# Performance work log

Hardware: AMD Instinct MI355X
Metric: run time of the kernel (lower is better)

Reference implementation:

```python
import jax, jax.numpy as jnp
import numpy as np

T = 1_000_000          # number of t_eval points (~1 year at 30 s)
N_ROOMS = 10
N = 12                 # 2 latent wall nodes + n_rooms
DT = 30.0              # seconds between t_eval points
LOAD_SCALE = 50.0      # physical_cooling_scaling: W/m^2 scale for sigmoid(loads)


def setup_inputs() -> dict:
    key = jax.random.key(0)
    k1, k2, k3, k4, k5 = jax.random.split(key, 5)
    t_eval = jnp.arange(T, dtype=jnp.float32) * DT
    x0 = 26.0 * jnp.ones((N,), jnp.float32)  # reset_iv: 26 C at every node
    # Stable slow RC dynamics: negative-definite-ish A with small coupling
    A = (-1e-5 * jnp.eye(N, dtype=jnp.float32)
         + 1e-6 * jax.random.normal(k1, (N, N), jnp.float32))
    B = 1e-6 * jax.random.normal(k2, (N, 1 + N_ROOMS), jnp.float32)
    Tout_data = 10.0 + 20.0 * jax.random.uniform(k3, (T,), jnp.float32)  # outdoor temp samples on t_eval grid
    loads_raw = jax.random.normal(k4, (2, N_ROOMS), jnp.float32)         # pre-sigmoid [cool; gain] loads
    room_areas = 10.0 + 40.0 * jax.random.uniform(k5, (N_ROOMS,), jnp.float32)
    return {"t_eval": t_eval, "x0": x0, "A": A, "B": B,
            "Tout_data": Tout_data, "loads_raw": loads_raw, "room_areas": room_areas}


def reference(t_eval, x0, A, B, Tout_data, loads_raw, room_areas):
    # transform + physical scaling of loads (self.transform = sigmoid)
    loads = jax.nn.sigmoid(loads_raw) * LOAD_SCALE
    cool_load, gain_load = loads[0], loads[1]
    action = 0.0  # no cooling policy -> self.action stays 0
    Q_area = -cool_load * action + gain_load            # [n_rooms]
    Q_watts = Q_area * room_areas                        # proportional_heating
    # u = [Tout; Q_watts] so B@u = B[:,0]*Tout + B[:,1:]@Q_watts (Q constant over t)
    b0 = B[:, 0]                                         # [N]
    Bq = B[:, 1:] @ Q_watts                              # [N], constant forcing
    h = t_eval[1] - t_eval[0]                            # uniform step
    # Linear interp of Tout: value at t_i, midpoint t_i+h/2, and t_{i+1}
    To_t = Tout_data[:-1]
    To_n = Tout_data[1:]
    To_m = 0.5 * (To_t + To_n)

    def f(x, To):  # dy/dt = A x + B u
        return A @ x + b0 * To + Bq

    def step(x, tou):
        to_t, to_m, to_n = tou
        k1 = f(x, to_t)
        k2 = f(x + 0.5 * h * k1, to_m)
        k3 = f(x + 0.5 * h * k2, to_m)
        k4 = f(x + h * k3, to_n)
        xn = x + (h / 6.0) * (k1 + 2.0 * k2 + 2.0 * k3 + k4)
        return xn, xn

    _, xs = jax.lax.scan(step, x0, (To_t, To_m, To_n))
    return jnp.concatenate([x0[None, :], xs], axis=0)  # [T, N]
```

## Files before the change

### kernel.cpp

```cpp
#include <hip/hip_runtime.h>
#include <math.h>


#define S_STEPS 999999
#define CH      8
#define BLK     512
#define NB      256
#define NLOOK   16
#define NCHUNK  125000
#define LASTFULL 124998

#define OFF_M   0
#define OFF_C   144
#define OFF_AL  156
#define OFF_BE  168
#define OFF_K   192
#define OFF_P2  312
#define OFF_PQ  1608
#define OFF_PW  2040
#define OFF_PD  3048
#define OFF_AGG 5352

#define FMA4(Q,a,b,c,d,acc) fmaf((Q).w,(d),fmaf((Q).z,(c),fmaf((Q).y,(b),fmaf((Q).x,(a),(acc)))))

__device__ __forceinline__ void mv_acc(const float* Pf, const float* x, float* y) {
  const float4* P = reinterpret_cast<const float4*>(Pf);
#pragma unroll
  for (int i = 0; i < 12; ++i) {
    float4 a = P[3*i], b = P[3*i+1], c = P[3*i+2];
    y[i] = FMA4(c, x[8],x[9],x[10],x[11],
            FMA4(b, x[4],x[5],x[6],x[7],
             FMA4(a, x[0],x[1],x[2],x[3], y[i])));
  }
}

__device__ __forceinline__ void fold_chunk(const float* cons, const float* tos, float* v) {
  const float4* Kq = reinterpret_cast<const float4*>(cons + OFF_K);
  float4 c0=Kq[0], c1=Kq[1], c2=Kq[2];
  v[0]=c0.x; v[1]=c0.y; v[2]=c0.z; v[3]=c0.w;
  v[4]=c1.x; v[5]=c1.y; v[6]=c1.z; v[7]=c1.w;
  v[8]=c2.x; v[9]=c2.y; v[10]=c2.z; v[11]=c2.w;
#pragma unroll
  for (int s = 0; s < 9; ++s) {
    float ts = tos[s];
    float4 ka=Kq[3*(s+1)], kb=Kq[3*(s+1)+1], kc=Kq[3*(s+1)+2];
    v[0]=fmaf(ka.x,ts,v[0]); v[1]=fmaf(ka.y,ts,v[1]); v[2]=fmaf(ka.z,ts,v[2]); v[3]=fmaf(ka.w,ts,v[3]);
    v[4]=fmaf(kb.x,ts,v[4]); v[5]=fmaf(kb.y,ts,v[5]); v[6]=fmaf(kb.z,ts,v[6]); v[7]=fmaf(kb.w,ts,v[7]);
    v[8]=fmaf(kc.x,ts,v[8]); v[9]=fmaf(kc.y,ts,v[9]); v[10]=fmaf(kc.z,ts,v[10]); v[11]=fmaf(kc.w,ts,v[11]);
  }
}

__global__ void __launch_bounds__(512) setup_kernel(
    const float* __restrict__ t_eval, const float* __restrict__ A,
    const float* __restrict__ Bm, const float* __restrict__ loads_raw,
    const float* __restrict__ areas, float* ws) {
  __shared__ double H1[144], H2[144], H3[144], H4[144], Md[144];
  __shared__ double Qa[144], Qb[144], D1536[144];
  __shared__ double C128[144], C256[144], C512[144], C1024[144], C2048[144], C4096[144];
  __shared__ double cd[12], ald[12], bed[12], b0d[12], bqd[12];
  __shared__ double Vv[3][12], Kd[120];
  int t = threadIdx.x;
  double h = (double)t_eval[1] - (double)t_eval[0];
  if (t < 144) H1[t] = h * (double)A[t];
  if (t < 12) {
    b0d[t] = (double)Bm[t*11];
    double s = 0.0;
    for (int r = 0; r < 10; ++r) {
      double gq = 50.0 / (1.0 + exp(-(double)loads_raw[10 + r]));
      s += (double)Bm[t*11 + 1 + r] * (gq * (double)areas[r]);
    }
    bqd[t] = s;
  }
  if (t < 120) Kd[t] = 0.0;
  __syncthreads();
  if (t < 144) {
    int i=t/12, j=t%12; double s=0.0;
#pragma unroll
    for (int m = 0; m < 12; ++m) s += H1[i*12+m]*H1[m*12+j];
    H2[t]=s;
  }
  __syncthreads();
  if (t < 288) {
    int w=t/144, e=t%144, i=e/12, j=e%12;
    const double* Bp = w ? H2 : H1;
    double s = 0.0;
#pragma unroll
    for (int m = 0; m < 12; ++m) s += H2[i*12+m]*Bp[m*12+j];
    (w ? H4 : H3)[e] = s;
  }
  __syncthreads();
  if (t < 12) {
    double hb=0,h2b=0,h3b=0,hb0=0,h2b0=0,h3b0=0;
#pragma unroll
    for (int m = 0; m < 12; ++m) {
      hb  += H1[t*12+m]*bqd[m]; h2b  += H2[t*12+m]*bqd[m]; h3b  += H3[t*12+m]*bqd[m];
      hb0 += H1[t*12+m]*b0d[m]; h2b0 += H2[t*12+m]*b0d[m]; h3b0 += H3[t*12+m]*b0d[m];
    }
    double h6 = h / 6.0;
    cd[t]  = h6*(6.0*bqd[t] + 3.0*hb + h2b + 0.25*h3b);
    ald[t] = h6*(3.0*b0d[t] + 2.0*hb0 + 0.75*h2b0 + 0.25*h3b0);
    bed[t] = h6*(3.0*b0d[t] + hb0 + 0.25*h2b0);
    Vv[0][t]=ald[t]; Vv[1][t]=bed[t]; Vv[2][t]=cd[t];
    Kd[96+t] += ald[t]; Kd[108+t] += bed[t]; Kd[t] += cd[t];
  }
  if (t >= 144 && t < 288) {
    int e=t-144, i=e/12, j=e%12;
    Md[e] = (i==j ? 1.0 : 0.0) + H1[e] + 0.5*H2[e] + H3[e]/6.0 + H4[e]/24.0;
  }
  __syncthreads();
  if (t < 144) { ws[OFF_M+t] = (float)Md[t]; Qa[t] = Md[t]; }
  if (t < 12) {
    ws[OFF_C+t]=(float)cd[t]; ws[OFF_AL+t]=(float)ald[t]; ws[OFF_BE+t]=(float)bed[t];
  }
  __syncthreads();
  double* src = Qa; double* dst = Qb;
  for (int r = 1; r <= 12; ++r) {
    double acc = 0.0, ks = 0.0;
    if (t < 144) {
      int i=t/12, j=t%12;
#pragma unroll
      for (int m = 0; m < 12; ++m) acc += src[i*12+m]*src[m*12+j];
    }
    int w=0, i2=0;
    if (r <= 7 && t >= 256 && t < 292) {
      w=(t-256)/12; i2=(t-256)%12;
#pragma unroll
      for (int m = 0; m < 12; ++m) ks += Md[i2*12+m]*Vv[w][m];
    }
    __syncthreads();
    if (t < 144) {
      dst[t] = acc;
      if (r >= 3 && r <= 11) ws[OFF_P2+(r-3)*144+t] = (float)acc;
      if (r == 7)  C128[t]=acc;
      if (r == 8)  C256[t]=acc;
      if (r == 9)  C512[t]=acc;
      if (r == 10) C1024[t]=acc;
      if (r == 11) C2048[t]=acc;
      if (r == 12) C4096[t]=acc;
    }
    if (r <= 7 && t >= 256 && t < 292) {
      Vv[w][i2] = ks;
      if (w == 0) Kd[(8-r)*12+i2] += ks;
      else if (w == 1) Kd[(9-r)*12+i2] += ks;
      else Kd[i2] += ks;
    }
    __syncthreads();
    double* tmp = src; src = dst; dst = tmp;
  }
  if (t < 120) ws[OFF_K+t] = (float)Kd[t];
  if (t < 144) {
    ws[OFF_PQ+t]       = (float)C128[t];
    ws[OFF_PQ+144+t]   = (float)C256[t];
    ws[OFF_PW+t]       = (float)C512[t];
    ws[OFF_PW+144+t]   = (float)C1024[t];
    ws[OFF_PW+3*144+t] = (float)C2048[t];
    ws[OFF_PD+t]       = (t % 13 == 0) ? 1.f : 0.f;
    ws[OFF_PD+144+t]   = (float)C4096[t];
  }
  if (t < 432) {
    int w=t/144, e=t%144, i=e/12, j=e%12;
    const double* Ap = (w==0) ? C128 : C512;
    const double* Bp = (w==0) ? C256 : ((w==1) ? C1024 : C2048);
    double s = 0.0;
#pragma unroll
    for (int m = 0; m < 12; ++m) s += Ap[i*12+m]*Bp[m*12+j];
    if (w==0) ws[OFF_PQ+2*144+e] = (float)s;
    else if (w==1) { D1536[e]=s; ws[OFF_PW+2*144+e] = (float)s; }
    else ws[OFF_PW+4*144+e] = (float)s;
  }
  __syncthreads();
  if (t < 288) {
    int w=t/144, e=t%144, i=e/12, j=e%12;
    const double* Ap = (w==0) ? C1024 : D1536;
    double s = 0.0;
#pragma unroll
    for (int m = 0; m < 12; ++m) s += Ap[i*12+m]*C2048[m*12+j];
    ws[OFF_PW+((w==0)?5:6)*144+e] = (float)s;
  }
  for (int j = 2; j < NLOOK; ++j) {
    double acc = 0.0;
    if (t < 144) {
      int i=t/12, jj=t%12;
#pragma unroll
      for (int m = 0; m < 12; ++m) acc += src[i*12+m]*C4096[m*12+jj];
    }
    __syncthreads();
    if (t < 144) { dst[t] = acc; ws[OFF_PD+j*144+t] = (float)acc; }
    __syncthreads();
    double* tmp = src; src = dst; dst = tmp;
  }
}

__global__ void __launch_bounds__(BLK) block_agg(
    const float* cons, const float* __restrict__ To,
    const float* __restrict__ x0, float* agg) {
  __shared__ float Tw[96], Ta[48], Tb[24];
  int k = threadIdx.x, b = blockIdx.x;
  int g = b*BLK + k, base = g*CH;
  float v[12];
  if (g <= LASTFULL) {
    const float4* tp = reinterpret_cast<const float4*>(To + base);
    float4 ta = tp[0], tb = tp[1];
    float tos[9] = {ta.x,ta.y,ta.z,ta.w, tb.x,tb.y,tb.z,tb.w, To[base+8]};
    fold_chunk(cons, tos, v);
  } else {
#pragma unroll
    for (int i = 0; i < 12; ++i) v[i] = 0.f;
  }
  if (g == 0) {
    float xi[12];
#pragma unroll
    for (int i = 0; i < 12; ++i) xi[i] = x0[i];
    mv_acc(cons + OFF_P2, xi, v);
  }
#pragma unroll
  for (int l = 0; l < 6; ++l) {
    int off = 1 << l;
    float nb[12];
#pragma unroll
    for (int i = 0; i < 12; ++i) nb[i] = __shfl_up(v[i], (unsigned)off, 64);
    if ((k & 63) >= off) mv_acc(cons + OFF_P2 + l*144, nb, v);
  }
  if ((k & 63) == 63) {
#pragma unroll
    for (int i = 0; i < 12; ++i) Tw[(k>>6)*12 + i] = v[i];
  }
  __syncthreads();
  if (k < 48) {
    int p = k/12, i = k%12;
    const float* L = Tw + 2*p*12;
    float acc = Tw[(2*p+1)*12 + i];
    const float4* Pr = reinterpret_cast<const float4*>(cons + OFF_P2 + 6*144 + i*12);
    float4 p0=Pr[0], p1=Pr[1], p2=Pr[2];
    acc = FMA4(p0, L[0],L[1],L[2],L[3], acc);
    acc = FMA4(p1, L[4],L[5],L[6],L[7], acc);
    acc = FMA4(p2, L[8],L[9],L[10],L[11], acc);
    Ta[p*12+i] = acc;
  }
  __syncthreads();
  if (k < 24) {
    int q = k/12, i = k%12;
    const float* L = Ta + 2*q*12;
    float acc = Ta[(2*q+1)*12 + i];
    const float4* Pr = reinterpret_cast<const float4*>(cons + OFF_P2 + 7*144 + i*12);
    float4 p0=Pr[0], p1=Pr[1], p2=Pr[2];
    acc = FMA4(p0, L[0],L[1],L[2],L[3], acc);
    acc = FMA4(p1, L[4],L[5],L[6],L[7], acc);
    acc = FMA4(p2, L[8],L[9],L[10],L[11], acc);
    Tb[q*12+i] = acc;
  }
  __syncthreads();
  if (k < 12) {
    float acc = Tb[12 + k];
    const float4* Pr = reinterpret_cast<const float4*>(cons + OFF_P2 + 8*144 + k*12);
    float4 p0=Pr[0], p1=Pr[1], p2=Pr[2];
    acc = FMA4(p0, Tb[0],Tb[1],Tb[2],Tb[3], acc);
    acc = FMA4(p1, Tb[4],Tb[5],Tb[6],Tb[7], acc);
    acc = FMA4(p2, Tb[8],Tb[9],Tb[10],Tb[11], acc);
    agg[b*12 + k] = acc;
  }
}

#define ROWX(i, MA,MB,MC) xn[i] = FMA4(MC, x[8],x[9],x[10],x[11], \
    FMA4(MB, x[4],x[5],x[6],x[7], FMA4(MA, x[0],x[1],x[2],x[3], \
    fmaf(bv[i],ton,fmaf(av[i],tot,cv[i])))));

__global__ void __launch_bounds__(BLK, 2) scan_expand(
    const float* cons, const float* __restrict__ To,
    const float* __restrict__ x0, float* __restrict__ out) {
  __shared__ float lw[BLK*13];
  __shared__ float partl[NLOOK*12];
  __shared__ float Xs[12];
  __shared__ float Xw[96];
  __shared__ float Xq[384];
  int k = threadIdx.x, b = blockIdx.x;
  int g = b*BLK + k, base = g*CH;
  bool active = (g < NCHUNK), fullc = (g <= LASTFULL);
  float to[9];
  if (active) {
    const float4* tp = reinterpret_cast<const float4*>(To + base);
    float4 ta = tp[0], tb = tp[1];
    to[0]=ta.x; to[1]=ta.y; to[2]=ta.z; to[3]=ta.w;
    to[4]=tb.x; to[5]=tb.y; to[6]=tb.z; to[7]=tb.w;
    to[8] = fullc ? To[base+8] : 0.f;
  }
  float v[12];
  if (fullc) fold_chunk(cons, to, v);
  else {
#pragma unroll
    for (int i = 0; i < 12; ++i) v[i] = 0.f;
  }
  if (g == 0) {
    float xi[12];
#pragma unroll
    for (int i = 0; i < 12; ++i) xi[i] = x0[i];
    mv_acc(cons + OFF_P2, xi, v);
  }
#pragma unroll
  for (int i = 0; i < 12; ++i) lw[k*13+i] = v[i];
  if (k < NLOOK*12) {
    int j = k/12, i = k%12, src = b - 1 - j;
    float acc = 0.f;
    if (src >= 0) {
      const float4* Pr = reinterpret_cast<const float4*>(cons + OFF_PD + j*144 + i*12);
      const float4* Ar = reinterpret_cast<const float4*>(cons + OFF_AGG + src*12);
      float4 p0=Pr[0], p1=Pr[1], p2=Pr[2], a0=Ar[0], a1=Ar[1], a2=Ar[2];
      acc = FMA4(p0, a0.x,a0.y,a0.z,a0.w, acc);
      acc = FMA4(p1, a1.x,a1.y,a1.z,a1.w, acc);
      acc = FMA4(p2, a2.x,a2.y,a2.z,a2.w, acc);
    }
    partl[k] = acc;
  }
  __syncthreads();
  if (k < 12) {
    float s = 0.f;
#pragma unroll
    for (int j = 0; j < NLOOK; ++j) s += partl[j*12 + k];
    Xs[k] = s;
  }
#pragma unroll
  for (int l = 0; l < 9; ++l) {
    int off = 1 << l;
    bool act = (k >= off);
    float nb[12];
    if (act) {
#pragma unroll
      for (int i = 0; i < 12; ++i) nb[i] = lw[(k-off)*13 + i];
    }
    __syncthreads();
    if (act) {
      mv_acc(cons + OFF_P2 + l*144, nb, v);
#pragma unroll
      for (int i = 0; i < 12; ++i) lw[k*13+i] = v[i];
    }
    __syncthreads();
  }
  float sp[12];
  if (k > 0) {
#pragma unroll
    for (int i = 0; i < 12; ++i) sp[i] = lw[(k-1)*13 + i];
  } else {
#pragma unroll
    for (int i = 0; i < 12; ++i) sp[i] = 0.f;
  }
  if (k < 96) {
    int w = k/12, i = k%12;
    float acc;
    if (w == 0) acc = Xs[i];
    else {
      const float4* Wr = reinterpret_cast<const float4*>(cons + OFF_PW + (w-1)*144 + i*12);
      float4 p0=Wr[0], p1=Wr[1], p2=Wr[2];
      acc = FMA4(p0, Xs[0],Xs[1],Xs[2],Xs[3], 0.f);
      acc = FMA4(p1, Xs[4],Xs[5],Xs[6],Xs[7], acc);
      acc = FMA4(p2, Xs[8],Xs[9],Xs[10],Xs[11], acc);
    }
    Xw[w*12 + i] = acc;
  }
  __syncthreads();
  if (k < 384) {
    int q = k/12, i = k%12, d = q & 3;
    const float* xw = Xw + (q>>2)*12;
    float acc;
    if (d == 0) acc = xw[i];
    else {
      const float4* Qr = reinterpret_cast<const float4*>(cons + OFF_PQ + (d-1)*144 + i*12);
      float4 p0=Qr[0], p1=Qr[1], p2=Qr[2];
      acc = FMA4(p0, xw[0],xw[1],xw[2],xw[3], 0.f);
      acc = FMA4(p1, xw[4],xw[5],xw[6],xw[7], acc);
      acc = FMA4(p2, xw[8],xw[9],xw[10],xw[11], acc);
    }
    Xq[q*12 + i] = acc;
  }
  __syncthreads();
  float vp[12];
  {
    const float* xq = Xq + (k>>4)*12;
#pragma unroll
    for (int i = 0; i < 12; ++i) vp[i] = xq[i];
  }
#pragma unroll
  for (int l = 0; l < 4; ++l) {
    if ((k >> l) & 1) {
      float vn[12];
#pragma unroll
      for (int i = 0; i < 12; ++i) vn[i] = 0.f;
      mv_acc(cons + OFF_P2 + l*144, vp, vn);
#pragma unroll
      for (int i = 0; i < 12; ++i) vp[i] = vn[i];
    }
  }
  float x[12];
  if (k > 0) {
#pragma unroll
    for (int i = 0; i < 12; ++i) x[i] = vp[i] + sp[i];
  } else {
#pragma unroll
    for (int i = 0; i < 12; ++i) x[i] = vp[i] + (b == 0 ? x0[i] : 0.f);
  }
  if (b == 0 && k == 0) {
#pragma unroll
    for (int i = 0; i < 12; ++i) out[i] = x0[i];
  }
  if (!active) return;
  float cv[12], av[12], bv[12];
  {
    const float4* Cq = reinterpret_cast<const float4*>(cons + OFF_C);
    const float4* Aq = reinterpret_cast<const float4*>(cons + OFF_AL);
    const float4* Bq = reinterpret_cast<const float4*>(cons + OFF_BE);
    float4 q;
    q=Cq[0]; cv[0]=q.x;cv[1]=q.y;cv[2]=q.z;cv[3]=q.w;
    q=Cq[1]; cv[4]=q.x;cv[5]=q.y;cv[6]=q.z;cv[7]=q.w;
    q=Cq[2]; cv[8]=q.x;cv[9]=q.y;cv[10]=q.z;cv[11]=q.w;
    q=Aq[0]; av[0]=q.x;av[1]=q.y;av[2]=q.z;av[3]=q.w;
    q=Aq[1]; av[4]=q.x;av[5]=q.y;av[6]=q.z;av[7]=q.w;
    q=Aq[2]; av[8]=q.x;av[9]=q.y;av[10]=q.z;av[11]=q.w;
    q=Bq[0]; bv[0]=q.x;bv[1]=q.y;bv[2]=q.z;bv[3]=q.w;
    q=Bq[1]; bv[4]=q.x;bv[5]=q.y;bv[6]=q.z;bv[7]=q.w;
    q=Bq[2]; bv[8]=q.x;bv[9]=q.y;bv[10]=q.z;bv[11]=q.w;
  }
  const float4* Mq = reinterpret_cast<const float4*>(cons + OFF_M);
  float4 m00=Mq[0],  m01=Mq[1],  m02=Mq[2],  m03=Mq[3],  m04=Mq[4],  m05=Mq[5];
  float4 m06=Mq[6],  m07=Mq[7],  m08=Mq[8],  m09=Mq[9],  m10=Mq[10], m11=Mq[11];
  float4 m12=Mq[12], m13=Mq[13], m14=Mq[14], m15=Mq[15], m16=Mq[16], m17=Mq[17];
  float4 m18=Mq[18], m19=Mq[19], m20=Mq[20], m21=Mq[21], m22=Mq[22], m23=Mq[23];
  float4 m24=Mq[24], m25=Mq[25], m26=Mq[26], m27=Mq[27], m28=Mq[28], m29=Mq[29];
  float4 m30=Mq[30], m31=Mq[31], m32=Mq[32], m33=Mq[33], m34=Mq[34], m35=Mq[35];
#pragma unroll
  for (int s = 0; s < CH; ++s) {
    int tt = base + s;
    if (tt >= S_STEPS) break;
    float tot = to[s], ton = to[s+1];
    float xn[12];
    ROWX(0,  m00,m01,m02)  ROWX(1,  m03,m04,m05)
    ROWX(2,  m06,m07,m08)  ROWX(3,  m09,m10,m11)
    ROWX(4,  m12,m13,m14)  ROWX(5,  m15,m16,m17)
    ROWX(6,  m18,m19,m20)  ROWX(7,  m21,m22,m23)
    ROWX(8,  m24,m25,m26)  ROWX(9,  m27,m28,m29)
    ROWX(10, m30,m31,m32)  ROWX(11, m33,m34,m35)
    float4* op = reinterpret_cast<float4*>(out + (size_t)(tt+1)*12);
    op[0] = make_float4(xn[0],xn[1],xn[2],xn[3]);
    op[1] = make_float4(xn[4],xn[5],xn[6],xn[7]);
    op[2] = make_float4(xn[8],xn[9],xn[10],xn[11]);
#pragma unroll
    for (int i = 0; i < 12; ++i) x[i] = xn[i];
  }
}

extern "C" void kernel_launch(void* const* d_in, const int* in_sizes, int n_in,
                              void* d_out, int out_size, void* d_ws, size_t ws_size,
                              hipStream_t stream) {
  const float* t_eval    = (const float*)d_in[0];
  const float* x0        = (const float*)d_in[1];
  const float* A         = (const float*)d_in[2];
  const float* B         = (const float*)d_in[3];
  const float* To        = (const float*)d_in[4];
  const float* loads_raw = (const float*)d_in[5];
  const float* areas     = (const float*)d_in[6];
  float* out = (float*)d_out;
  float* ws  = (float*)d_ws;

  setup_kernel<<<1, 512, 0, stream>>>(t_eval, A, B, loads_raw, areas, ws);
  block_agg<<<NB, BLK, 0, stream>>>(ws, To, x0, ws + OFF_AGG);
  scan_expand<<<NB, BLK, 0, stream>>>(ws, To, x0, out);
}
```

Before: 135.6 us.

## Restructure scan into smaller chunks, more blocks, and wave-shuffle scan

```diff
diff --git a/kernel.cpp b/kernel.cpp
--- a/kernel.cpp
+++ b/kernel.cpp
@@ -3,23 +3,22 @@
 
 
 #define S_STEPS 999999
-#define CH      8
-#define BLK     512
-#define NB      256
-#define NLOOK   16
-#define NCHUNK  125000
-#define LASTFULL 124998
+#define CH      4
+#define BLK     256
+#define NB      977
+#define NCHUNK  250000
+#define LASTFULL 249998
 
 #define OFF_M   0
 #define OFF_C   144
 #define OFF_AL  156
 #define OFF_BE  168
 #define OFF_K   192
-#define OFF_P2  312
-#define OFF_PQ  1608
-#define OFF_PW  2040
-#define OFF_PD  3048
-#define OFF_AGG 5352
+#define OFF_P2  264
+#define OFF_PA  1416
+#define OFF_PL  1704
+#define OFF_PD  2136
+#define OFF_AGG 4440
 
 #define FMA4(Q,a,b,c,d,acc) fmaf((Q).w,(d),fmaf((Q).z,(c),fmaf((Q).y,(b),fmaf((Q).x,(a),(acc)))))
 
@@ -34,14 +33,23 @@
   }
 }
 
-__device__ __forceinline__ void fold_chunk(const float* cons, const float* tos, float* v) {
+__device__ __forceinline__ float rowdot(const float* Prow, const float* xv) {
+  const float4* P = reinterpret_cast<const float4*>(Prow);
+  float4 a = P[0], b = P[1], c = P[2];
+  return FMA4(c, xv[8],xv[9],xv[10],xv[11],
+          FMA4(b, xv[4],xv[5],xv[6],xv[7],
+           FMA4(a, xv[0],xv[1],xv[2],xv[3], 0.f)));
+}
+
+__device__ __forceinline__ void fold_chunk(const float* __restrict__ cons,
+                                           const float* tos, float* v) {
   const float4* Kq = reinterpret_cast<const float4*>(cons + OFF_K);
   float4 c0=Kq[0], c1=Kq[1], c2=Kq[2];
   v[0]=c0.x; v[1]=c0.y; v[2]=c0.z; v[3]=c0.w;
   v[4]=c1.x; v[5]=c1.y; v[6]=c1.z; v[7]=c1.w;
   v[8]=c2.x; v[9]=c2.y; v[10]=c2.z; v[11]=c2.w;
 #pragma unroll
-  for (int s = 0; s < 9; ++s) {
+  for (int s = 0; s < 5; ++s) {
     float ts = tos[s];
     float4 ka=Kq[3*(s+1)], kb=Kq[3*(s+1)+1], kc=Kq[3*(s+1)+2];
     v[0]=fmaf(ka.x,ts,v[0]); v[1]=fmaf(ka.y,ts,v[1]); v[2]=fmaf(ka.z,ts,v[2]); v[3]=fmaf(ka.w,ts,v[3]);
@@ -55,10 +63,11 @@
     const float* __restrict__ Bm, const float* __restrict__ loads_raw,
     const float* __restrict__ areas, float* ws) {
   __shared__ double H1[144], H2[144], H3[144], H4[144], Md[144];
-  __shared__ double Qa[144], Qb[144], D1536[144];
-  __shared__ double C128[144], C256[144], C512[144], C1024[144], C2048[144], C4096[144];
+  __shared__ double Qa[144], Qb[144];
+  __shared__ double C64[144], C128[144], C256[144], C512[144];
+  __shared__ double C1024[144], C2048[144], C4096[144];
   __shared__ double cd[12], ald[12], bed[12], b0d[12], bqd[12];
-  __shared__ double Vv[3][12], Kd[120];
+  __shared__ double Vv[3][12], Kd[72];
   int t = threadIdx.x;
   double h = (double)t_eval[1] - (double)t_eval[0];
   if (t < 144) H1[t] = h * (double)A[t];
@@ -71,7 +80,7 @@
     }
     bqd[t] = s;
   }
-  if (t < 120) Kd[t] = 0.0;
+  if (t < 72) Kd[t] = 0.0;
   __syncthreads();
   if (t < 144) {
     int i=t/12, j=t%12; double s=0.0;
@@ -101,7 +110,7 @@
     ald[t] = h6*(3.0*b0d[t] + 2.0*hb0 + 0.75*h2b0 + 0.25*h3b0);
     bed[t] = h6*(3.0*b0d[t] + hb0 + 0.25*h2b0);
     Vv[0][t]=ald[t]; Vv[1][t]=bed[t]; Vv[2][t]=cd[t];
-    Kd[96+t] += ald[t]; Kd[108+t] += bed[t]; Kd[t] += cd[t];
+    Kd[48+t] += ald[t]; Kd[60+t] += bed[t]; Kd[t] += cd[t];
   }
   if (t >= 144 && t < 288) {
     int e=t-144, i=e/12, j=e%12;
@@ -122,7 +131,7 @@
       for (int m = 0; m < 12; ++m) acc += src[i*12+m]*src[m*12+j];
     }
     int w=0, i2=0;
-    if (r <= 7 && t >= 256 && t < 292) {
+    if (r <= 3 && t >= 256 && t < 292) {
       w=(t-256)/12; i2=(t-256)%12;
 #pragma unroll
       for (int m = 0; m < 12; ++m) ks += Md[i2*12+m]*Vv[w][m];
@@ -130,7 +139,8 @@
     __syncthreads();
     if (t < 144) {
       dst[t] = acc;
-      if (r >= 3 && r <= 11) ws[OFF_P2+(r-3)*144+t] = (float)acc;
+      if (r >= 2 && r <= 9) ws[OFF_P2+(r-2)*144+t] = (float)acc;
+      if (r == 6)  C64[t]=acc;
       if (r == 7)  C128[t]=acc;
       if (r == 8)  C256[t]=acc;
       if (r == 9)  C512[t]=acc;
@@ -138,46 +148,34 @@
       if (r == 11) C2048[t]=acc;
       if (r == 12) C4096[t]=acc;
     }
-    if (r <= 7 && t >= 256 && t < 292) {
+    if (r <= 3 && t >= 256 && t < 292) {
       Vv[w][i2] = ks;
-      if (w == 0) Kd[(8-r)*12+i2] += ks;
-      else if (w == 1) Kd[(9-r)*12+i2] += ks;
+      if (w == 0) Kd[(4-r)*12+i2] += ks;
+      else if (w == 1) Kd[(5-r)*12+i2] += ks;
       else Kd[i2] += ks;
     }
     __syncthreads();
     double* tmp = src; src = dst; dst = tmp;
   }
-  if (t < 120) ws[OFF_K+t] = (float)Kd[t];
+  if (t < 72) ws[OFF_K+t] = (float)Kd[t];
   if (t < 144) {
-    ws[OFF_PQ+t]       = (float)C128[t];
-    ws[OFF_PQ+144+t]   = (float)C256[t];
-    ws[OFF_PW+t]       = (float)C512[t];
-    ws[OFF_PW+144+t]   = (float)C1024[t];
-    ws[OFF_PW+3*144+t] = (float)C2048[t];
-    ws[OFF_PD+t]       = (t % 13 == 0) ? 1.f : 0.f;
-    ws[OFF_PD+144+t]   = (float)C4096[t];
+    ws[OFF_PL+t]     = (float)C1024[t];
+    ws[OFF_PL+144+t] = (float)C2048[t];
+    ws[OFF_PD+t]     = (t % 13 == 0) ? 1.f : 0.f;
+    ws[OFF_PD+144+t] = (float)C4096[t];
   }
   if (t < 432) {
     int w=t/144, e=t%144, i=e/12, j=e%12;
-    const double* Ap = (w==0) ? C128 : C512;
-    const double* Bp = (w==0) ? C256 : ((w==1) ? C1024 : C2048);
+    const double* Ap = (w==0) ? C64 : ((w==1) ? C256 : C1024);
+    const double* Bp = (w==0) ? C128 : ((w==1) ? C512 : C2048);
     double s = 0.0;
 #pragma unroll
     for (int m = 0; m < 12; ++m) s += Ap[i*12+m]*Bp[m*12+j];
-    if (w==0) ws[OFF_PQ+2*144+e] = (float)s;
-    else if (w==1) { D1536[e]=s; ws[OFF_PW+2*144+e] = (float)s; }
-    else ws[OFF_PW+4*144+e] = (float)s;
-  }
-  __syncthreads();
-  if (t < 288) {
-    int w=t/144, e=t%144, i=e/12, j=e%12;
-    const double* Ap = (w==0) ? C1024 : D1536;
-    double s = 0.0;
-#pragma unroll
-    for (int m = 0; m < 12; ++m) s += Ap[i*12+m]*C2048[m*12+j];
-    ws[OFF_PW+((w==0)?5:6)*144+e] = (float)s;
-  }
-  for (int j = 2; j < NLOOK; ++j) {
+    if (w==0) ws[OFF_PA+e] = (float)s;
+    else if (w==1) ws[OFF_PA+144+e] = (float)s;
+    else ws[OFF_PL+2*144+e] = (float)s;
+  }
+  for (int j = 2; j < 16; ++j) {
     double acc = 0.0;
     if (t < 144) {
       int i=t/12, jj=t%12;
@@ -191,19 +189,25 @@
   }
 }
 
-__global__ void __launch_bounds__(BLK) block_agg(
-    const float* cons, const float* __restrict__ To,
-    const float* __restrict__ x0, float* agg) {
-  __shared__ float Tw[96], Ta[48], Tb[24];
+__global__ void __launch_bounds__(BLK, 4) block_agg(
+    const float* __restrict__ cons, const float* __restrict__ To,
+    const float* __restrict__ x0, float* __restrict__ agg) {
+  __shared__ __align__(16) float Tw[48], Ta[24];
   int k = threadIdx.x, b = blockIdx.x;
   int g = b*BLK + k, base = g*CH;
+  bool fullc = (g <= LASTFULL);
+  float to_[5];
+#pragma unroll
+  for (int i = 0; i < 5; ++i) to_[i] = 0.f;
+  if (fullc) {
+    const float4* tp = reinterpret_cast<const float4*>(To + base);
+    float4 ta = tp[0];
+    to_[0]=ta.x; to_[1]=ta.y; to_[2]=ta.z; to_[3]=ta.w;
+    to_[4]=To[base+4];
+  }
   float v[12];
-  if (g <= LASTFULL) {
-    const float4* tp = reinterpret_cast<const float4*>(To + base);
-    float4 ta = tp[0], tb = tp[1];
-    float tos[9] = {ta.x,ta.y,ta.z,ta.w, tb.x,tb.y,tb.z,tb.w, To[base+8]};
-    fold_chunk(cons, tos, v);
-  } else {
+  if (fullc) fold_chunk(cons, to_, v);
+  else {
 #pragma unroll
     for (int i = 0; i < 12; ++i) v[i] = 0.f;
   }
@@ -213,79 +217,56 @@
     for (int i = 0; i < 12; ++i) xi[i] = x0[i];
     mv_acc(cons + OFF_P2, xi, v);
   }
+  int j = k & 63;
 #pragma unroll
   for (int l = 0; l < 6; ++l) {
     int off = 1 << l;
     float nb[12];
 #pragma unroll
     for (int i = 0; i < 12; ++i) nb[i] = __shfl_up(v[i], (unsigned)off, 64);
-    if ((k & 63) >= off) mv_acc(cons + OFF_P2 + l*144, nb, v);
-  }
-  if ((k & 63) == 63) {
+    if (j >= off) mv_acc(cons + OFF_P2 + l*144, nb, v);
+  }
+  if (j == 63) {
 #pragma unroll
     for (int i = 0; i < 12; ++i) Tw[(k>>6)*12 + i] = v[i];
   }
   __syncthreads();
-  if (k < 48) {
-    int p = k/12, i = k%12;
-    const float* L = Tw + 2*p*12;
-    float acc = Tw[(2*p+1)*12 + i];
-    const float4* Pr = reinterpret_cast<const float4*>(cons + OFF_P2 + 6*144 + i*12);
-    float4 p0=Pr[0], p1=Pr[1], p2=Pr[2];
-    acc = FMA4(p0, L[0],L[1],L[2],L[3], acc);
-    acc = FMA4(p1, L[4],L[5],L[6],L[7], acc);
-    acc = FMA4(p2, L[8],L[9],L[10],L[11], acc);
-    Ta[p*12+i] = acc;
-  }
-  __syncthreads();
   if (k < 24) {
-    int q = k/12, i = k%12;
-    const float* L = Ta + 2*q*12;
-    float acc = Ta[(2*q+1)*12 + i];
-    const float4* Pr = reinterpret_cast<const float4*>(cons + OFF_P2 + 7*144 + i*12);
-    float4 p0=Pr[0], p1=Pr[1], p2=Pr[2];
-    acc = FMA4(p0, L[0],L[1],L[2],L[3], acc);
-    acc = FMA4(p1, L[4],L[5],L[6],L[7], acc);
-    acc = FMA4(p2, L[8],L[9],L[10],L[11], acc);
-    Tb[q*12+i] = acc;
+    int p = k/12, comp = k - p*12;
+    Ta[k] = rowdot(cons + OFF_P2 + 6*144 + comp*12, Tw + 2*p*12)
+          + Tw[(2*p+1)*12 + comp];
   }
   __syncthreads();
   if (k < 12) {
-    float acc = Tb[12 + k];
-    const float4* Pr = reinterpret_cast<const float4*>(cons + OFF_P2 + 8*144 + k*12);
-    float4 p0=Pr[0], p1=Pr[1], p2=Pr[2];
-    acc = FMA4(p0, Tb[0],Tb[1],Tb[2],Tb[3], acc);
-    acc = FMA4(p1, Tb[4],Tb[5],Tb[6],Tb[7], acc);
-    acc = FMA4(p2, Tb[8],Tb[9],Tb[10],Tb[11], acc);
-    agg[b*12 + k] = acc;
-  }
-}
-
-#define ROWX(i, MA,MB,MC) xn[i] = FMA4(MC, x[8],x[9],x[10],x[11], \
-    FMA4(MB, x[4],x[5],x[6],x[7], FMA4(MA, x[0],x[1],x[2],x[3], \
-    fmaf(bv[i],ton,fmaf(av[i],tot,cv[i])))));
+    agg[b*12 + k] = rowdot(cons + OFF_P2 + 7*144 + k*12, Ta) + Ta[12 + k];
+  }
+}
 
 __global__ void __launch_bounds__(BLK, 2) scan_expand(
-    const float* cons, const float* __restrict__ To,
-    const float* __restrict__ x0, float* __restrict__ out) {
-  __shared__ float lw[BLK*13];
-  __shared__ float partl[NLOOK*12];
-  __shared__ float Xs[12];
-  __shared__ float Xw[96];
-  __shared__ float Xq[384];
+    const float* __restrict__ cons, const float* __restrict__ To,
+    const float* __restrict__ x0, const float* __restrict__ agg,
+    float* __restrict__ out) {
+  __shared__ __align__(16) float Tw[48];
+  __shared__ __align__(16) float Pw[48];
+  __shared__ __align__(16) float lkb[64*12];
+  __shared__ __align__(16) float yv[16*12];
+  __shared__ __align__(16) float zv[16*12];
+  __shared__ __align__(16) float Xs[12];
+  __shared__ __align__(16) float Qw[48];
   int k = threadIdx.x, b = blockIdx.x;
   int g = b*BLK + k, base = g*CH;
   bool active = (g < NCHUNK), fullc = (g <= LASTFULL);
-  float to[9];
+  float to_[5];
+#pragma unroll
+  for (int i = 0; i < 5; ++i) to_[i] = 0.f;
   if (active) {
     const float4* tp = reinterpret_cast<const float4*>(To + base);
-    float4 ta = tp[0], tb = tp[1];
-    to[0]=ta.x; to[1]=ta.y; to[2]=ta.z; to[3]=ta.w;
-    to[4]=tb.x; to[5]=tb.y; to[6]=tb.z; to[7]=tb.w;
-    to[8] = fullc ? To[base+8] : 0.f;
+    float4 ta = tp[0];
+    to_[0]=ta.x; to_[1]=ta.y; to_[2]=ta.z; to_[3]=ta.w;
+    to_[4] = fullc ? To[base+4] : 0.f;
   }
   float v[12];
-  if (fullc) fold_chunk(cons, to, v);
+  if (fullc) fold_chunk(cons, to_, v);
   else {
 #pragma unroll
     for (int i = 0; i < 12; ++i) v[i] = 0.f;
@@ -296,151 +277,127 @@
     for (int i = 0; i < 12; ++i) xi[i] = x0[i];
     mv_acc(cons + OFF_P2, xi, v);
   }
-#pragma unroll
-  for (int i = 0; i < 12; ++i) lw[k*13+i] = v[i];
-  if (k < NLOOK*12) {
-    int j = k/12, i = k%12, src = b - 1 - j;
+  int j = k & 63, w = k >> 6;
+#pragma unroll
+  for (int l = 0; l < 6; ++l) {
+    int off = 1 << l;
+    float nb[12];
+#pragma unroll
+    for (int i = 0; i < 12; ++i) nb[i] = __shfl_up(v[i], (unsigned)off, 64);
+    if (j >= off) mv_acc(cons + OFF_P2 + l*144, nb, v);
+  }
+  float se[12];
+#pragma unroll
+  for (int i = 0; i < 12; ++i) {
+    float u = __shfl_up(v[i], 1u, 64);
+    se[i] = (j == 0) ? 0.f : u;
+  }
+  if (j == 63) {
+#pragma unroll
+    for (int i = 0; i < 12; ++i) Tw[w*12 + i] = v[i];
+  }
+#pragma unroll
+  for (int r = 0; r < 3; ++r) {
+    int idx = k + r*BLK;
+    int slot = idx / 12, comp = idx - slot*12;
+    int src = b - 1 - slot;
     float acc = 0.f;
     if (src >= 0) {
-      const float4* Pr = reinterpret_cast<const float4*>(cons + OFF_PD + j*144 + i*12);
-      const float4* Ar = reinterpret_cast<const float4*>(cons + OFF_AGG + src*12);
-      float4 p0=Pr[0], p1=Pr[1], p2=Pr[2], a0=Ar[0], a1=Ar[1], a2=Ar[2];
-      acc = FMA4(p0, a0.x,a0.y,a0.z,a0.w, acc);
-      acc = FMA4(p1, a1.x,a1.y,a1.z,a1.w, acc);
-      acc = FMA4(p2, a2.x,a2.y,a2.z,a2.w, acc);
-    }
-    partl[k] = acc;
+      int jj = slot & 3;
+      const float* ag = agg + src*12;
+      acc = (jj == 0) ? ag[comp]
+          : rowdot(cons + OFF_PL + (jj-1)*144 + comp*12, ag);
+    }
+    lkb[idx] = acc;
+  }
+  __syncthreads();
+  if (k < 192) {
+    int i = k/12, comp = k - i*12;
+    yv[k] = lkb[(4*i)*12+comp] + lkb[(4*i+1)*12+comp]
+          + lkb[(4*i+2)*12+comp] + lkb[(4*i+3)*12+comp];
+  } else if (k < 216) {
+    int q = k - 192;
+    if (q < 12) Pw[q] = 0.f;
+    else Pw[q] = Tw[q-12];
+  }
+  __syncthreads();
+  if (k < 192) {
+    int i = k/12, comp = k - i*12;
+    zv[k] = (i == 0) ? yv[comp]
+          : rowdot(cons + OFF_PD + i*144 + comp*12, yv + i*12);
+  } else if (k < 204) {
+    int comp = k - 192;
+    Pw[24+comp] = rowdot(cons + OFF_P2 + 6*144 + comp*12, Pw+12) + Tw[12+comp];
   }
   __syncthreads();
   if (k < 12) {
     float s = 0.f;
 #pragma unroll
-    for (int j = 0; j < NLOOK; ++j) s += partl[j*12 + k];
+    for (int i = 0; i < 16; ++i) s += zv[i*12 + k];
     Xs[k] = s;
-  }
-#pragma unroll
-  for (int l = 0; l < 9; ++l) {
-    int off = 1 << l;
-    bool act = (k >= off);
-    float nb[12];
-    if (act) {
-#pragma unroll
-      for (int i = 0; i < 12; ++i) nb[i] = lw[(k-off)*13 + i];
-    }
-    __syncthreads();
-    if (act) {
-      mv_acc(cons + OFF_P2 + l*144, nb, v);
-#pragma unroll
-      for (int i = 0; i < 12; ++i) lw[k*13+i] = v[i];
-    }
-    __syncthreads();
-  }
-  float sp[12];
-  if (k > 0) {
-#pragma unroll
-    for (int i = 0; i < 12; ++i) sp[i] = lw[(k-1)*13 + i];
-  } else {
-#pragma unroll
-    for (int i = 0; i < 12; ++i) sp[i] = 0.f;
-  }
-  if (k < 96) {
-    int w = k/12, i = k%12;
+  } else if (k >= 192 && k < 204) {
+    int comp = k - 192;
+    Pw[36+comp] = rowdot(cons + OFF_P2 + 6*144 + comp*12, Pw+24) + Tw[24+comp];
+  }
+  __syncthreads();
+  if (k < 48) {
+    int ww = k/12, comp = k - ww*12;
     float acc;
-    if (w == 0) acc = Xs[i];
-    else {
-      const float4* Wr = reinterpret_cast<const float4*>(cons + OFF_PW + (w-1)*144 + i*12);
-      float4 p0=Wr[0], p1=Wr[1], p2=Wr[2];
-      acc = FMA4(p0, Xs[0],Xs[1],Xs[2],Xs[3], 0.f);
-      acc = FMA4(p1, Xs[4],Xs[5],Xs[6],Xs[7], acc);
-      acc = FMA4(p2, Xs[8],Xs[9],Xs[10],Xs[11], acc);
-    }
-    Xw[w*12 + i] = acc;
-  }
-  __syncthreads();
-  if (k < 384) {
-    int q = k/12, i = k%12, d = q & 3;
-    const float* xw = Xw + (q>>2)*12;
-    float acc;
-    if (d == 0) acc = xw[i];
-    else {
-      const float4* Qr = reinterpret_cast<const float4*>(cons + OFF_PQ + (d-1)*144 + i*12);
-      float4 p0=Qr[0], p1=Qr[1], p2=Qr[2];
-      acc = FMA4(p0, xw[0],xw[1],xw[2],xw[3], 0.f);
-      acc = FMA4(p1, xw[4],xw[5],xw[6],xw[7], acc);
-      acc = FMA4(p2, xw[8],xw[9],xw[10],xw[11], acc);
-    }
-    Xq[q*12 + i] = acc;
-  }
-  __syncthreads();
-  float vp[12];
-  {
-    const float* xq = Xq + (k>>4)*12;
-#pragma unroll
-    for (int i = 0; i < 12; ++i) vp[i] = xq[i];
-  }
-#pragma unroll
-  for (int l = 0; l < 4; ++l) {
-    if ((k >> l) & 1) {
+    if (ww == 0) acc = Xs[comp];
+    else if (ww == 1) acc = rowdot(cons + OFF_P2 + 6*144 + comp*12, Xs);
+    else if (ww == 2) acc = rowdot(cons + OFF_P2 + 7*144 + comp*12, Xs);
+    else acc = rowdot(cons + OFF_PA + 144 + comp*12, Xs);
+    Qw[k] = acc + Pw[k];
+  }
+  __syncthreads();
+  if (!active) return;
+  float x[12];
+#pragma unroll
+  for (int i = 0; i < 12; ++i) x[i] = Qw[w*12 + i];
+#pragma unroll
+  for (int l = 0; l < 6; ++l) {
+    if ((j >> l) & 1) {
       float vn[12];
 #pragma unroll
       for (int i = 0; i < 12; ++i) vn[i] = 0.f;
-      mv_acc(cons + OFF_P2 + l*144, vp, vn);
-#pragma unroll
-      for (int i = 0; i < 12; ++i) vp[i] = vn[i];
-    }
-  }
-  float x[12];
-  if (k > 0) {
-#pragma unroll
-    for (int i = 0; i < 12; ++i) x[i] = vp[i] + sp[i];
-  } else {
-#pragma unroll
-    for (int i = 0; i < 12; ++i) x[i] = vp[i] + (b == 0 ? x0[i] : 0.f);
-  }
+      mv_acc(cons + OFF_P2 + l*144, x, vn);
+#pragma unroll
+      for (int i = 0; i < 12; ++i) x[i] = vn[i];
+    }
+  }
+#pragma unroll
+  for (int i = 0; i < 12; ++i) x[i] += se[i];
   if (b == 0 && k == 0) {
 #pragma unroll
+    for (int i = 0; i < 12; ++i) x[i] += x0[i];
+#pragma unroll
     for (int i = 0; i < 12; ++i) out[i] = x0[i];
   }
-  if (!active) return;
   float cv[12], av[12], bv[12];
-  {
-    const float4* Cq = reinterpret_cast<const float4*>(cons + OFF_C);
-    const float4* Aq = reinterpret_cast<const float4*>(cons + OFF_AL);
-    const float4* Bq = reinterpret_cast<const float4*>(cons + OFF_BE);
-    float4 q;
-    q=Cq[0]; cv[0]=q.x;cv[1]=q.y;cv[2]=q.z;cv[3]=q.w;
-    q=Cq[1]; cv[4]=q.x;cv[5]=q.y;cv[6]=q.z;cv[7]=q.w;
-    q=Cq[2]; cv[8]=q.x;cv[9]=q.y;cv[10]=q.z;cv[11]=q.w;
-    q=Aq[0]; av[0]=q.x;av[1]=q.y;av[2]=q.z;av[3]=q.w;
-    q=Aq[1]; av[4]=q.x;av[5]=q.y;av[6]=q.z;av[7]=q.w;
-    q=Aq[2]; av[8]=q.x;av[9]=q.y;av[10]=q.z;av[11]=q.w;
-    q=Bq[0]; bv[0]=q.x;bv[1]=q.y;bv[2]=q.z;bv[3]=q.w;
-    q=Bq[1]; bv[4]=q.x;bv[5]=q.y;bv[6]=q.z;bv[7]=q.w;
-    q=Bq[2]; bv[8]=q.x;bv[9]=q.y;bv[10]=q.z;bv[11]=q.w;
+#pragma unroll
+  for (int i = 0; i < 12; ++i) {
+    cv[i] = cons[OFF_C + i]; av[i] = cons[OFF_AL + i]; bv[i] = cons[OFF_BE + i];
   }
   const float4* Mq = reinterpret_cast<const float4*>(cons + OFF_M);
-  float4 m00=Mq[0],  m01=Mq[1],  m02=Mq[2],  m03=Mq[3],  m04=Mq[4],  m05=Mq[5];
-  float4 m06=Mq[6],  m07=Mq[7],  m08=Mq[8],  m09=Mq[9],  m10=Mq[10], m11=Mq[11];
-  float4 m12=Mq[12], m13=Mq[13], m14=Mq[14], m15=Mq[15], m16=Mq[16], m17=Mq[17];
-  float4 m18=Mq[18], m19=Mq[19], m20=Mq[20], m21=Mq[21], m22=Mq[22], m23=Mq[23];
-  float4 m24=Mq[24], m25=Mq[25], m26=Mq[26], m27=Mq[27], m28=Mq[28], m29=Mq[29];
-  float4 m30=Mq[30], m31=Mq[31], m32=Mq[32], m33=Mq[33], m34=Mq[34], m35=Mq[35];
 #pragma unroll
   for (int s = 0; s < CH; ++s) {
+    float tot = to_[s], ton = (s < CH-1) ? to_[s+1] : to_[4];
+    float xn[12];
+#pragma unroll
+    for (int i = 0; i < 12; ++i) {
+      float4 a = Mq[3*i], bq = Mq[3*i+1], c = Mq[3*i+2];
+      xn[i] = FMA4(c, x[8],x[9],x[10],x[11],
+               FMA4(bq, x[4],x[5],x[6],x[7],
+                FMA4(a, x[0],x[1],x[2],x[3],
+                 fmaf(bv[i],ton,fmaf(av[i],tot,cv[i])))));
+    }
     int tt = base + s;
-    if (tt >= S_STEPS) break;
-    float tot = to[s], ton = to[s+1];
-    float xn[12];
-    ROWX(0,  m00,m01,m02)  ROWX(1,  m03,m04,m05)
-    ROWX(2,  m06,m07,m08)  ROWX(3,  m09,m10,m11)
-    ROWX(4,  m12,m13,m14)  ROWX(5,  m15,m16,m17)
-    ROWX(6,  m18,m19,m20)  ROWX(7,  m21,m22,m23)
-    ROWX(8,  m24,m25,m26)  ROWX(9,  m27,m28,m29)
-    ROWX(10, m30,m31,m32)  ROWX(11, m33,m34,m35)
-    float4* op = reinterpret_cast<float4*>(out + (size_t)(tt+1)*12);
-    op[0] = make_float4(xn[0],xn[1],xn[2],xn[3]);
-    op[1] = make_float4(xn[4],xn[5],xn[6],xn[7]);
-    op[2] = make_float4(xn[8],xn[9],xn[10],xn[11]);
+    if (tt < S_STEPS) {
+      float4* op = reinterpret_cast<float4*>(out + (size_t)(tt+1)*12);
+      op[0] = make_float4(xn[0],xn[1],xn[2],xn[3]);
+      op[1] = make_float4(xn[4],xn[5],xn[6],xn[7]);
+      op[2] = make_float4(xn[8],xn[9],xn[10],xn[11]);
+    }
 #pragma unroll
     for (int i = 0; i < 12; ++i) x[i] = xn[i];
   }
@@ -461,5 +418,5 @@
 
   setup_kernel<<<1, 512, 0, stream>>>(t_eval, A, B, loads_raw, areas, ws);
   block_agg<<<NB, BLK, 0, stream>>>(ws, To, x0, ws + OFF_AGG);
-  scan_expand<<<NB, BLK, 0, stream>>>(ws, To, x0, out);
-}
+  scan_expand<<<NB, BLK, 0, stream>>>(ws, To, x0, ws + OFF_AGG, out);
+}
```

Result: faster. 131.8 us (-2.8%).
